# Kernel tuning notes

Hardware: AMD Instinct MI355X
Metric: run time of the kernel (lower is better)

## Reference

```python
import jax, jax.numpy as jnp
import numpy as np

B, N, C_IN = 4, 2048, 64
HID, HEADS, NQ = 128, 4, 16
D = HID // HEADS  # per-head dim = 32
NEG_SLOPE = 0.2
MASK_VAL = -1e9


def setup_inputs() -> dict:
    key = jax.random.key(0)
    ks = jax.random.split(key, 8)
    x = jax.random.normal(ks[0], (B, N, C_IN), dtype=jnp.float32)
    adj = jax.random.randint(ks[1], (N, N), 0, 2, dtype=jnp.int32)
    # lin_in: Linear(in_channels, hidden_dim)
    W_in = jax.random.normal(ks[2], (C_IN, HID), dtype=jnp.float32) / np.sqrt(C_IN)
    b_in = jnp.zeros((HID,), dtype=jnp.float32)
    # attention vectors [1, heads, d]
    att_src = jax.random.normal(ks[3], (1, HEADS, D), dtype=jnp.float32) * 0.1
    att_dst = jax.random.normal(ks[4], (1, HEADS, D), dtype=jnp.float32) * 0.1
    # output_head: Linear(num_nodes*hidden_dim, num_qubits)
    W_out = jax.random.normal(ks[5], (N * HID, NQ), dtype=jnp.float32) / np.sqrt(N * HID)
    b_out = jnp.zeros((NQ,), dtype=jnp.float32)
    return {"x": x, "adj": adj, "W_in": W_in, "b_in": b_in,
            "att_src": att_src, "att_dst": att_dst,
            "W_out": W_out, "b_out": b_out}


def reference(x, adj, W_in, b_in, att_src, att_dst, W_out, b_out):
    b, n, _ = x.shape
    h = (x @ W_in + b_in).reshape(b, n, HEADS, D)          # [B,N,H,D]
    alpha_src = jnp.sum(h * att_src, axis=-1)               # [B,N,H]
    alpha_dst = jnp.sum(h * att_dst, axis=-1)               # [B,N,H]
    # additive scores: score[b,i,j,h] = src[b,i,h] + dst[b,j,h]
    scores = alpha_src[:, :, None, :] + alpha_dst[:, None, :, :]  # [B,N,N,H]
    scores = jnp.where(scores >= 0, scores, NEG_SLOPE * scores)   # leaky relu
    mask = (adj == 0)[None, :, :, None]                     # [1,N,N,1]
    scores = jnp.where(mask, MASK_VAL, scores)
    alpha = jax.nn.softmax(scores, axis=2)                  # softmax over neighbors j
    # dropout p=0.0 (eval) -> identity
    out = jnp.einsum('bijh,bjhd->bihd', alpha, h)           # [B,N,H,D]
    out = out.reshape(b, n * HEADS * D)                     # [B, N*HID]
    return out @ W_out + b_out                              # [B, NQ]
```

## Files before the change

### kernel.cpp

```cpp
#include <hip/hip_runtime.h>
#include <math.h>

#define BB 4
#define NN 2048
#define CIN 64
#define HID 128
#define HEADS 4
#define NQ 16
#define KTOT (NN*HID)
#define LOG2E 1.44269504088896340736f
#define NEGBIG_BITS 0xC2C80000u
#define NSL 4

typedef __attribute__((ext_vector_type(8))) _Float16 half8;
typedef __attribute__((ext_vector_type(4))) float f32x4;
typedef __attribute__((ext_vector_type(4))) unsigned uint4v;

__global__ __launch_bounds__(256) void k_hidden(
    const float* __restrict__ x, const float* __restrict__ W_in,
    const float* __restrict__ b_in, const float* __restrict__ att_src,
    const float* __restrict__ att_dst, _Float16* __restrict__ hHT,
    float* __restrict__ srcA, float* __restrict__ dstA)
{
    __shared__ float Wl[CIN * HID];
    __shared__ float xl[16][CIN];
    const int t = threadIdx.x;
    const int jj0 = blockIdx.x * 16;

    {
        const float4* Ws = (const float4*)W_in;
        float4* Wd = (float4*)Wl;
#pragma unroll
        for (int u = 0; u < 8; ++u) Wd[t + 256 * u] = Ws[t + 256 * u];
        ((float4*)&xl[0][0])[t] = ((const float4*)(x + (size_t)jj0 * CIN))[t];
    }
    __syncthreads();

    const int c = t & 127, rg = t >> 7;
    const int b = jj0 >> 11, j0 = (jj0 & (NN - 1)) + rg * 8;
    const int h = c >> 5;

    float acc[8];
    const float bc = b_in[c];
#pragma unroll
    for (int rr = 0; rr < 8; ++rr) acc[rr] = bc;

#pragma unroll
    for (int k4 = 0; k4 < CIN; k4 += 4) {
        const float w0 = Wl[(k4 + 0) * HID + c];
        const float w1 = Wl[(k4 + 1) * HID + c];
        const float w2 = Wl[(k4 + 2) * HID + c];
        const float w3 = Wl[(k4 + 3) * HID + c];
#pragma unroll
        for (int rr = 0; rr < 8; ++rr) {
            const float4 xv = *(const float4*)&xl[rg * 8 + rr][k4];
            acc[rr] = fmaf(xv.w, w3, fmaf(xv.z, w2, fmaf(xv.y, w1, fmaf(xv.x, w0, acc[rr]))));
        }
    }

    half8 hv;
#pragma unroll
    for (int rr = 0; rr < 8; ++rr) hv[rr] = (_Float16)acc[rr];
    *(half8*)(hHT + (size_t)b * KTOT + (size_t)(j0 >> 5) * 4096 + c * 32 + (j0 & 31)) = hv;

    const float as = att_src[c], ad = att_dst[c];
#pragma unroll
    for (int rr = 0; rr < 8; ++rr) {
        float vs = acc[rr] * as, vd = acc[rr] * ad;
#pragma unroll
        for (int m = 16; m >= 1; m >>= 1) {
            vs += __shfl_xor(vs, m, 64);
            vd += __shfl_xor(vd, m, 64);
        }
        if ((t & 31) == 0) {
            srcA[(size_t)(b * HEADS + h) * NN + j0 + rr] = vs * LOG2E;
            dstA[(size_t)(b * HEADS + h) * NN + j0 + rr] = vd * LOG2E;
        }
    }
}

__global__ __launch_bounds__(256) void k_adjb(const int* __restrict__ adj,
                                              unsigned* __restrict__ adjT,
                                              const float* __restrict__ b_out,
                                              float* __restrict__ dout)
{
    const int t = threadIdx.x;
    if (blockIdx.x == 0 && t < 64) dout[t] = b_out[t & 15];
    const int gid = blockIdx.x * 256 + t;
    const int lane = t & 63;
    const int4* p = (const int4*)(adj + (size_t)gid * 8);
    const int4 a = p[0], b = p[1];
    unsigned byte =
        (a.x != 0 ? 1u : 0u)  | (a.y != 0 ? 2u : 0u)  | (a.z != 0 ? 4u : 0u)  | (a.w != 0 ? 8u : 0u) |
        (b.x != 0 ? 16u : 0u) | (b.y != 0 ? 32u : 0u) | (b.z != 0 ? 64u : 0u) | (b.w != 0 ? 128u : 0u);
    unsigned u = byte | (((unsigned)__shfl_xor((int)byte, 1, 64)) << 8);
    u = u | (((unsigned)__shfl_xor((int)u, 2, 64)) << 16);
    if ((lane & 3) == 0) {
        const int widx = gid >> 2;
        const int i = widx >> 6, jw = widx & 63;
        adjT[(size_t)jw * NN + i] = u;
    }
}

__global__ __launch_bounds__(256, 5) void k_attn(
    const unsigned* __restrict__ adjT, const _Float16* __restrict__ hHT,
    const float* __restrict__ srcA, const float* __restrict__ dstA,
    float* __restrict__ P, float* __restrict__ S)
{
    const int t = threadIdx.x;
    const int lane = t & 63;
    const int h = t >> 6;
    const int bx = blockIdx.x;
    const int iq = bx & 127;
    const int b = (bx >> 7) & 3;
    const int jq = bx >> 9;
    const int i0 = iq * 16;
    const int jb0 = jq * 16;

    const int r16 = lane & 15;
    const int g = lane >> 4;

    const float srci = srcA[(size_t)(b * HEADS + h) * NN + i0 + r16];
    const unsigned* adjr = adjT + (size_t)jb0 * NN + i0 + r16;
    const _Float16* hb = hHT + (size_t)b * KTOT + (size_t)jb0 * 4096
                             + (h * 32 + r16) * 32 + g * 8;
    const float4* dst4 = (const float4*)(dstA + (size_t)(b * HEADS + h) * NN + jq * 512) + 2 * g;

    f32x4 acc0 = {0.f, 0.f, 0.f, 0.f};
    f32x4 acc1 = {0.f, 0.f, 0.f, 0.f};
    f32x4 accS = {0.f, 0.f, 0.f, 0.f};
    const half8 ones = {(_Float16)1.f, (_Float16)1.f, (_Float16)1.f, (_Float16)1.f,
                        (_Float16)1.f, (_Float16)1.f, (_Float16)1.f, (_Float16)1.f};

#pragma unroll 1
    for (int n = 0; n < 16; ++n) {
        const unsigned word = adjr[(size_t)n * NN];
        const half8 bb0 = *(const half8*)(hb + n * 4096);
        const half8 bb1 = *(const half8*)(hb + n * 4096 + 512);
        const float4 dv0 = dst4[n * 8];
        const float4 dv1 = dst4[n * 8 + 1];

        const unsigned bits = word >> (8 * g);
        const float dvv[8] = {dv0.x, dv0.y, dv0.z, dv0.w, dv1.x, dv1.y, dv1.z, dv1.w};
        float wv[8];
#pragma unroll
        for (int e = 0; e < 8; ++e) {
            float s = srci + dvv[e];
            s = fmaxf(s, 0.2f * s);
            const unsigned m = (unsigned)(((int)(bits << (31 - e))) >> 31);
            const unsigned su = __builtin_bit_cast(unsigned, s);
            wv[e] = __builtin_amdgcn_exp2f(
                __builtin_bit_cast(float, (su & m) | (NEGBIG_BITS & ~m)));
        }
        uint4v uu;
        uu[0] = __builtin_bit_cast(unsigned, __builtin_amdgcn_cvt_pkrtz(wv[0], wv[1]));
        uu[1] = __builtin_bit_cast(unsigned, __builtin_amdgcn_cvt_pkrtz(wv[2], wv[3]));
        uu[2] = __builtin_bit_cast(unsigned, __builtin_amdgcn_cvt_pkrtz(wv[4], wv[5]));
        uu[3] = __builtin_bit_cast(unsigned, __builtin_amdgcn_cvt_pkrtz(wv[6], wv[7]));
        const half8 af = __builtin_bit_cast(half8, uu);
        acc0 = __builtin_amdgcn_mfma_f32_16x16x32_f16(af, bb0, acc0, 0, 0, 0);
        acc1 = __builtin_amdgcn_mfma_f32_16x16x32_f16(af, bb1, acc1, 0, 0, 0);
        accS = __builtin_amdgcn_mfma_f32_16x16x32_f16(af, ones, accS, 0, 0, 0);
    }

    const size_t prow0 = (size_t)(jq * BB + b) * NN + i0;
#pragma unroll
    for (int r = 0; r < 4; ++r) {
        const size_t row = prow0 + 4 * g + r;
        P[row * HID + h * 32 + r16]      = acc0[r];
        P[row * HID + h * 32 + 16 + r16] = acc1[r];
        if (r16 == 0) S[row * HEADS + h] = accS[r];
    }
}

__global__ __launch_bounds__(256) void k_proj(
    const float* __restrict__ P, const float* __restrict__ S,
    const float* __restrict__ W_out, float* __restrict__ dout)
{
    __shared__ float wlT[NQ][260];
    __shared__ float red[256];

    const int t = threadIdx.x;
    const int k0 = blockIdx.x * 256;

#pragma unroll
    for (int u = 0; u < 4; ++u) {
        const int flat = (u * 256 + t) * 4;
        const float4 wv = *(const float4*)(W_out + (size_t)k0 * NQ + flat);
        const int krel = flat >> 4;
        const int q0 = flat & 15;
        wlT[q0 + 0][krel] = wv.x;
        wlT[q0 + 1][krel] = wv.y;
        wlT[q0 + 2][krel] = wv.z;
        wlT[q0 + 3][krel] = wv.w;
    }
    __syncthreads();

    const int q = t & 15;
    const int b = (t >> 4) & 3;
    const int ks = (t >> 6) * 64;
    const int i = (k0 + ks) >> 7;

    const float* p0 = P + (size_t)(0 * BB + b) * KTOT + k0 + ks;
    const float* p1 = P + (size_t)(1 * BB + b) * KTOT + k0 + ks;
    const float* p2 = P + (size_t)(2 * BB + b) * KTOT + k0 + ks;
    const float* p3 = P + (size_t)(3 * BB + b) * KTOT + k0 + ks;

    float acc = 0.f;
#pragma unroll
    for (int seg = 0; seg < 2; ++seg) {
        const int h = ((k0 + ks + seg * 32) >> 5) & 3;
        float rs = 0.f;
#pragma unroll
        for (int s = 0; s < NSL; ++s)
            rs += S[((size_t)(s * BB + b) * NN + i) * HEADS + h];
        const float inv = __builtin_amdgcn_rcpf(rs);
#pragma unroll
        for (int k4 = 0; k4 < 8; ++k4) {
            const int kk = seg * 32 + k4 * 4;
            const float4 a0 = *(const float4*)(p0 + kk);
            const float4 a1 = *(const float4*)(p1 + kk);
            const float4 a2 = *(const float4*)(p2 + kk);
            const float4 a3 = *(const float4*)(p3 + kk);
            const float4 wq = *(const float4*)&wlT[q][ks + kk];
            acc = fmaf(((a0.x + a1.x) + (a2.x + a3.x)) * inv, wq.x, acc);
            acc = fmaf(((a0.y + a1.y) + (a2.y + a3.y)) * inv, wq.y, acc);
            acc = fmaf(((a0.z + a1.z) + (a2.z + a3.z)) * inv, wq.z, acc);
            acc = fmaf(((a0.w + a1.w) + (a2.w + a3.w)) * inv, wq.w, acc);
        }
    }

    red[t] = acc;
    __syncthreads();
    if (t < 64)
        atomicAdd(&dout[t], red[t] + red[t + 64] + red[t + 128] + red[t + 192]);
}

extern "C" void kernel_launch(void* const* d_in, const int* in_sizes, int n_in,
                              void* d_out, int out_size, void* d_ws, size_t ws_size,
                              hipStream_t stream)
{
    const float* x       = (const float*)d_in[0];
    const int*   adj     = (const int*)d_in[1];
    const float* W_in    = (const float*)d_in[2];
    const float* b_in    = (const float*)d_in[3];
    const float* att_src = (const float*)d_in[4];
    const float* att_dst = (const float*)d_in[5];
    const float* W_out   = (const float*)d_in[6];
    const float* b_out   = (const float*)d_in[7];
    float* out = (float*)d_out;

    float* P    = (float*)d_ws;
    float* S    = P + (size_t)NSL * BB * KTOT;
    float* srcA = S + (size_t)NSL * BB * NN * HEADS;
    float* dstA = srcA + (size_t)BB * HEADS * NN;
    _Float16* hHT = (_Float16*)(dstA + (size_t)BB * HEADS * NN);
    unsigned* adjT = (unsigned*)((char*)hHT + sizeof(_Float16) * (size_t)BB * KTOT);

    k_hidden<<<BB * NN / 16, 256, 0, stream>>>(x, W_in, b_in, att_src, att_dst, hHT, srcA, dstA);
    k_adjb<<<NN * NN / 8 / 256, 256, 0, stream>>>(adj, adjT, b_out, out);
    k_attn<<<NSL * BB * (NN / 16), 256, 0, stream>>>(adjT, hHT, srcA, dstA, P, S);
    k_proj<<<KTOT / 256, 256, 0, stream>>>(P, S, W_out, out);
}
```

Measured before the change: 79.66 us.

## Process two 16-row query tiles per attention block to reuse B-operand loads

The attention kernel now handles 32 query rows per block instead of 16, so the h (B operand) fragments and dst scores loaded each iteration feed two sets of MFMAs. This halves the number of blocks and the redundant global loads of hHT and dstA, and a sched_barrier groups the loads ahead of the compute. In exchange register pressure rises (six accumulators), so occupancy is lowered to 4 blocks per CU and the grid shrinks to 1024 blocks.

Result: faster. 74.58 us (-6.4%).

```diff
diff --git a/kernel.cpp b/kernel.cpp
--- a/kernel.cpp
+++ b/kernel.cpp
@@ -102,7 +102,7 @@
     }
 }
 
-__global__ __launch_bounds__(256, 5) void k_attn(
+__global__ __launch_bounds__(256, 4) void k_attn(
     const unsigned* __restrict__ adjT, const _Float16* __restrict__ hHT,
     const float* __restrict__ srcA, const float* __restrict__ dstA,
     float* __restrict__ P, float* __restrict__ S)
@@ -111,37 +111,33 @@
     const int lane = t & 63;
     const int h = t >> 6;
     const int bx = blockIdx.x;
-    const int iq = bx & 127;
-    const int b = (bx >> 7) & 3;
-    const int jq = bx >> 9;
-    const int i0 = iq * 16;
+    const int iq = bx & 63;
+    const int b = (bx >> 6) & 3;
+    const int jq = bx >> 8;
+    const int i0 = iq * 32;
     const int jb0 = jq * 16;
 
     const int r16 = lane & 15;
     const int g = lane >> 4;
 
-    const float srci = srcA[(size_t)(b * HEADS + h) * NN + i0 + r16];
-    const unsigned* adjr = adjT + (size_t)jb0 * NN + i0 + r16;
+    const float srci0 = srcA[(size_t)(b * HEADS + h) * NN + i0 + r16];
+    const float srci1 = srcA[(size_t)(b * HEADS + h) * NN + i0 + 16 + r16];
+    const unsigned* adjr0 = adjT + (size_t)jb0 * NN + i0 + r16;
+    const unsigned* adjr1 = adjr0 + 16;
     const _Float16* hb = hHT + (size_t)b * KTOT + (size_t)jb0 * 4096
                              + (h * 32 + r16) * 32 + g * 8;
     const float4* dst4 = (const float4*)(dstA + (size_t)(b * HEADS + h) * NN + jq * 512) + 2 * g;
 
-    f32x4 acc0 = {0.f, 0.f, 0.f, 0.f};
-    f32x4 acc1 = {0.f, 0.f, 0.f, 0.f};
-    f32x4 accS = {0.f, 0.f, 0.f, 0.f};
+    f32x4 acc00 = {0.f, 0.f, 0.f, 0.f};
+    f32x4 acc01 = {0.f, 0.f, 0.f, 0.f};
+    f32x4 acc10 = {0.f, 0.f, 0.f, 0.f};
+    f32x4 acc11 = {0.f, 0.f, 0.f, 0.f};
+    f32x4 accS0 = {0.f, 0.f, 0.f, 0.f};
+    f32x4 accS1 = {0.f, 0.f, 0.f, 0.f};
     const half8 ones = {(_Float16)1.f, (_Float16)1.f, (_Float16)1.f, (_Float16)1.f,
                         (_Float16)1.f, (_Float16)1.f, (_Float16)1.f, (_Float16)1.f};
 
-#pragma unroll 1
-    for (int n = 0; n < 16; ++n) {
-        const unsigned word = adjr[(size_t)n * NN];
-        const half8 bb0 = *(const half8*)(hb + n * 4096);
-        const half8 bb1 = *(const half8*)(hb + n * 4096 + 512);
-        const float4 dv0 = dst4[n * 8];
-        const float4 dv1 = dst4[n * 8 + 1];
-
-        const unsigned bits = word >> (8 * g);
-        const float dvv[8] = {dv0.x, dv0.y, dv0.z, dv0.w, dv1.x, dv1.y, dv1.z, dv1.w};
+    auto MAKEAF = [&](float srci, unsigned bits, const float* dvv) -> half8 {
         float wv[8];
 #pragma unroll
         for (int e = 0; e < 8; ++e) {
@@ -157,19 +153,43 @@
         uu[1] = __builtin_bit_cast(unsigned, __builtin_amdgcn_cvt_pkrtz(wv[2], wv[3]));
         uu[2] = __builtin_bit_cast(unsigned, __builtin_amdgcn_cvt_pkrtz(wv[4], wv[5]));
         uu[3] = __builtin_bit_cast(unsigned, __builtin_amdgcn_cvt_pkrtz(wv[6], wv[7]));
-        const half8 af = __builtin_bit_cast(half8, uu);
-        acc0 = __builtin_amdgcn_mfma_f32_16x16x32_f16(af, bb0, acc0, 0, 0, 0);
-        acc1 = __builtin_amdgcn_mfma_f32_16x16x32_f16(af, bb1, acc1, 0, 0, 0);
-        accS = __builtin_amdgcn_mfma_f32_16x16x32_f16(af, ones, accS, 0, 0, 0);
+        return __builtin_bit_cast(half8, uu);
+    };
+
+#pragma unroll 1
+    for (int n = 0; n < 16; ++n) {
+        const unsigned w0 = adjr0[(size_t)n * NN];
+        const unsigned w1 = adjr1[(size_t)n * NN];
+        const half8 bb0 = *(const half8*)(hb + n * 4096);
+        const half8 bb1 = *(const half8*)(hb + n * 4096 + 512);
+        const float4 dv0 = dst4[n * 8];
+        const float4 dv1 = dst4[n * 8 + 1];
+        __builtin_amdgcn_sched_barrier(0);
+
+        const float dvv[8] = {dv0.x, dv0.y, dv0.z, dv0.w, dv1.x, dv1.y, dv1.z, dv1.w};
+        const half8 af0 = MAKEAF(srci0, w0 >> (8 * g), dvv);
+        const half8 af1 = MAKEAF(srci1, w1 >> (8 * g), dvv);
+        acc00 = __builtin_amdgcn_mfma_f32_16x16x32_f16(af0, bb0, acc00, 0, 0, 0);
+        acc01 = __builtin_amdgcn_mfma_f32_16x16x32_f16(af0, bb1, acc01, 0, 0, 0);
+        accS0 = __builtin_amdgcn_mfma_f32_16x16x32_f16(af0, ones, accS0, 0, 0, 0);
+        acc10 = __builtin_amdgcn_mfma_f32_16x16x32_f16(af1, bb0, acc10, 0, 0, 0);
+        acc11 = __builtin_amdgcn_mfma_f32_16x16x32_f16(af1, bb1, acc11, 0, 0, 0);
+        accS1 = __builtin_amdgcn_mfma_f32_16x16x32_f16(af1, ones, accS1, 0, 0, 0);
     }
 
     const size_t prow0 = (size_t)(jq * BB + b) * NN + i0;
 #pragma unroll
     for (int r = 0; r < 4; ++r) {
-        const size_t row = prow0 + 4 * g + r;
-        P[row * HID + h * 32 + r16]      = acc0[r];
-        P[row * HID + h * 32 + 16 + r16] = acc1[r];
-        if (r16 == 0) S[row * HEADS + h] = accS[r];
+        const size_t row0 = prow0 + 4 * g + r;
+        const size_t row1 = prow0 + 16 + 4 * g + r;
+        P[row0 * HID + h * 32 + r16]      = acc00[r];
+        P[row0 * HID + h * 32 + 16 + r16] = acc01[r];
+        P[row1 * HID + h * 32 + r16]      = acc10[r];
+        P[row1 * HID + h * 32 + 16 + r16] = acc11[r];
+        if (r16 == 0) {
+            S[row0 * HEADS + h] = accS0[r];
+            S[row1 * HEADS + h] = accS1[r];
+        }
     }
 }
 
@@ -259,6 +279,6 @@
 
     k_hidden<<<BB * NN / 16, 256, 0, stream>>>(x, W_in, b_in, att_src, att_dst, hHT, srcA, dstA);
     k_adjb<<<NN * NN / 8 / 256, 256, 0, stream>>>(adj, adjT, b_out, out);
-    k_attn<<<NSL * BB * (NN / 16), 256, 0, stream>>>(adjT, hHT, srcA, dstA, P, S);
+    k_attn<<<NSL * BB * (NN / 32), 256, 0, stream>>>(adjT, hHT, srcA, dstA, P, S);
     k_proj<<<KTOT / 256, 256, 0, stream>>>(P, S, W_out, out);
 }
```
